# Optimization experiments

Measured on AMD Instinct MI355X. Metric: run time of the kernel, lower is better.

Reference implementation:

```python
import jax, jax.numpy as jnp
from jax import lax
import numpy as np

B = 128
EPS = 1e-5


def _local_conv(x, w, b, kh, kw, sh, sw):
    # x: [B, C, H, W]; w: [nkh, nkw, O, C, kh, kw]; b: [O, nkh, nkw]
    nkh, nkw = w.shape[0], w.shape[1]
    # gather strided patches: [B, C, nkh, nkw, kh, kw]
    pats = jnp.stack([
        jnp.stack([
            x[:, :, di:di + sh * (nkh - 1) + 1:sh, dj:dj + sw * (nkw - 1) + 1:sw]
            for dj in range(kw)], axis=-1)
        for di in range(kh)], axis=-2)
    # per-location (unshared) contraction
    out = jnp.einsum('bchwkl,hwockl->bohw', pats, w)
    return out + b[None]


def _flatten_into_2d(o):
    # [B, O, h, w] -> [B, 1, r*h, r*w] with r = sqrt(O), channel-vector tiled as rxr block
    b, oc, h, w = o.shape
    r = int(round(oc ** 0.5))
    y = o.transpose(0, 2, 3, 1).reshape(b, h, w, r, r)
    y = y.transpose(0, 1, 3, 2, 4).reshape(b, r * h, r * w)
    return y[:, None]


def _layernorm2d(x, g, bta):
    # normalize over last two dims (torch nn.LayerNorm([H, W]))
    m = jnp.mean(x, axis=(-2, -1), keepdims=True)
    v = jnp.mean((x - m) ** 2, axis=(-2, -1), keepdims=True)
    return (x - m) * lax.rsqrt(v + EPS) * g + bta


def _maxpool2(x):
    return lax.reduce_window(x, -jnp.inf, lax.max, (1, 1, 2, 2), (1, 1, 2, 2), 'VALID')


def setup_inputs() -> dict:
    key = jax.random.key(0)
    ks = jax.random.split(key, 5)
    x = jax.random.normal(ks[0], (B, 3, 224, 224), jnp.float32)
    # xavier-normal-ish std for each per-location weight
    w0 = jax.random.normal(ks[1], (55, 55, 16, 3, 8, 8), jnp.float32) * 0.0406
    b0 = jnp.zeros((16, 55, 55), jnp.float32)
    g0 = jnp.ones((220, 220), jnp.float32)
    be0 = jnp.zeros((220, 220), jnp.float32)
    w1 = jax.random.normal(ks[2], (53, 53, 9, 1, 6, 6), jnp.float32) * 0.074
    b1 = jnp.zeros((9, 53, 53), jnp.float32)
    g1 = jnp.ones((159, 159), jnp.float32)
    be1 = jnp.zeros((159, 159), jnp.float32)
    fcw = jax.random.normal(ks[3], (1000, 25281), jnp.float32) * 0.01
    fcb = jnp.zeros((1000,), jnp.float32)
    return {"x": x, "w0": w0, "b0": b0, "g0": g0, "be0": be0,
            "w1": w1, "b1": b1, "g1": g1, "be1": be1, "fcw": fcw, "fcb": fcb}


def reference(x, w0, b0, g0, be0, w1, b1, g1, be1, fcw, fcb):
    # layer 0 (locally connected, padding 0): [B,16,55,55] -> 2D map [B,1,220,220]
    h = _local_conv(x, w0, b0, 8, 8, 4, 4)
    h = _flatten_into_2d(h)
    h = _layernorm2d(jax.nn.relu(h), g0, be0)
    h = _maxpool2(h)  # [B,1,110,110]  (i==0 -> pool; dropout is identity in eval)
    # layer 1: [B,9,53,53] -> [B,1,159,159]; i==1 odd -> no pool
    h = _local_conv(h, w1, b1, 6, 6, 2, 2)
    h = _flatten_into_2d(h)
    h = _layernorm2d(jax.nn.relu(h), g1, be1)
    logits = h.reshape(h.shape[0], -1) @ fcw.T + fcb
    return jax.nn.softmax(logits, axis=1)
```

## Files before the change

kernel.cpp:

```cpp
#include <hip/hip_runtime.h>


typedef __attribute__((ext_vector_type(8))) short short8;
typedef __attribute__((ext_vector_type(4))) float float4v;

__device__ __forceinline__ short f2bf(float f) {
    unsigned u = __float_as_uint(f);
    u += 0x7FFFu + ((u >> 16) & 1u);
    return (short)(u >> 16);
}

__global__ __launch_bounds__(256, 4) void k_conv0(const float* __restrict__ x,
                                                  const float* __restrict__ w0,
                                                  const float* __restrict__ b0,
                                                  float* __restrict__ y0)
{
    __shared__ float xs[2][20 * 132];
    __shared__ float wsd[2][512];

    const int t = threadIdx.x;
    const int orig = blockIdx.x;
    const int xcd = orig & 7, lin = orig >> 3;
    const int bid = (xcd < 2 ? xcd * 97 : 194 + (xcd - 2) * 96) + lin;
    const int tw = bid / 55;
    const int oh = bid % 55;
    const bool lastT = (tw == 13);

    const float* xrow0 = x + (oh << 2) * 224 + (tw << 4);
    const float* wbase = w0 + (oh * 55 + (tw << 2)) * 3072;

    int sb[3], sc[3], gsc[3];
    #pragma unroll
    for (int i = 0; i < 3; ++i) {
        int q = t + (i << 8);
        sb[i] = q / 5;
        sc[i] = q - sb[i] * 5;
        gsc[i] = (lastT && sc[i] > 3) ? 3 : sc[i];
    }
    const int nq = (t < 128) ? 3 : 2;

    const int wlm  = t >> 5;
    const int wom  = (t & 31) >> 1;
    const int whm  = t & 1;
    const bool wact = (t < 128);
    const int wl_l = ((tw << 2) + wlm > 54) ? 0 : wlm;
    const float* wq_base = wbase + wl_l * 3072 + wom * 192 + (whm << 2);

    const int bq = t & 31;
    const int oq = (t >> 5) & 3;
    const int lp = t >> 7;

    float4 xv[3];
    float4 wv = make_float4(0.f, 0.f, 0.f, 0.f);
    #pragma unroll
    for (int i = 0; i < 3; ++i)
        if (i < nq) xv[i] = *(const float4*)(xrow0 + sb[i] * 150528 + (gsc[i] << 2));
    if (wact) wv = *(const float4*)(wq_base);

    float acc[2][4][4] = {};

    #pragma unroll 2
    for (int k = 0; k < 24; ++k) {
        float* xb = xs[k & 1];
        float* wb = wsd[k & 1];
        #pragma unroll
        for (int i = 0; i < 3; ++i) {
            if (i < nq) {
                float* d = xb + (sc[i] << 2) * 132 + sb[i];
                d[0] = xv[i].x; d[132] = xv[i].y; d[264] = xv[i].z; d[396] = xv[i].w;
            }
        }
        if (wact) {
            float* d = wb + (wlm << 7) + (whm << 6) + wom;
            d[0] = wv.x; d[16] = wv.y; d[32] = wv.z; d[48] = wv.w;
        }
        if (k < 23) {
            const int kn = k + 1;
            const int ch = kn >> 3, rw = kn & 7;
            const float* xr = xrow0 + ch * 50176 + rw * 224;
            #pragma unroll
            for (int i = 0; i < 3; ++i)
                if (i < nq) xv[i] = *(const float4*)(xr + sb[i] * 150528 + (gsc[i] << 2));
            if (wact) wv = *(const float4*)(wq_base + (ch << 6) + (rw << 3));
        }
        __syncthreads();
        #pragma unroll
        for (int i = 0; i < 2; ++i) {
            const int l = (lp << 1) + i;
            #pragma unroll
            for (int kc = 0; kc < 8; ++kc) {
                float4 xq = *(const float4*)(xb + ((l << 2) + kc) * 132 + (bq << 2));
                float4 wq = *(const float4*)(wb + (l << 7) + (kc << 4) + (oq << 2));
                const float xr4[4] = {xq.x, xq.y, xq.z, xq.w};
                const float wr4[4] = {wq.x, wq.y, wq.z, wq.w};
                #pragma unroll
                for (int b4 = 0; b4 < 4; ++b4)
                    #pragma unroll
                    for (int j = 0; j < 4; ++j)
                        acc[i][b4][j] += xr4[b4] * wr4[j];
            }
        }
    }

    #pragma unroll
    for (int i = 0; i < 2; ++i) {
        const int l = (lp << 1) + i;
        const int ow = (tw << 2) + l;
        if (ow < 55) {
            const int loc = oh * 55 + ow;
            float bias[4];
            #pragma unroll
            for (int j = 0; j < 4; ++j)
                bias[j] = b0[((oq << 2) + j) * 3025 + loc];
            float* ybase = y0 + ((oh << 2) + oq) * 220 + (ow << 2);
            #pragma unroll
            for (int b4 = 0; b4 < 4; ++b4) {
                const int b = (bq << 2) + b4;
                float ov[4];
                #pragma unroll
                for (int j = 0; j < 4; ++j) {
                    float v = acc[i][b4][j] + bias[j];
                    ov[j] = v > 0.f ? v : 0.f;
                }
                float4 o4;
                o4.x = ov[0]; o4.y = ov[1]; o4.z = ov[2]; o4.w = ov[3];
                *(float4*)(ybase + b * 48400) = o4;
            }
        }
    }
}

__global__ void k_stats(const float* __restrict__ src, float2* __restrict__ stats, int count)
{
    const int b = blockIdx.x, t = threadIdx.x;
    const float* p = src + (long)b * count;
    const int nq = count >> 2;
    float s = 0.f, s2 = 0.f;
    for (int i = t; i < nq; i += 256) {
        float4 v = *(const float4*)(p + (i << 2));
        s  += (v.x + v.y) + (v.z + v.w);
        s2 += (v.x * v.x + v.y * v.y) + (v.z * v.z + v.w * v.w);
    }
    if (t == 0 && (count & 3)) {
        for (int i = nq << 2; i < count; ++i) { float v = p[i]; s += v; s2 += v * v; }
    }
    #pragma unroll
    for (int off = 32; off > 0; off >>= 1) {
        s  += __shfl_down(s,  off, 64);
        s2 += __shfl_down(s2, off, 64);
    }
    __shared__ float rs[4], rs2[4];
    if ((t & 63) == 0) { rs[t >> 6] = s; rs2[t >> 6] = s2; }
    __syncthreads();
    if (t == 0) {
        float S  = rs[0] + rs[1] + rs[2] + rs[3];
        float S2 = rs2[0] + rs2[1] + rs2[2] + rs2[3];
        float m  = S / count;
        float var = S2 / count - m * m;
        stats[b] = make_float2(m, rsqrtf(var + 1e-5f));
    }
}

__global__ void k_pool(const float* __restrict__ y0, const float2* __restrict__ st,
                       const float* __restrict__ g0, const float* __restrict__ be0,
                       float* __restrict__ P)
{
    int idx = blockIdx.x * 256 + threadIdx.x;
    if (idx >= 128 * 110 * 110) return;
    int b = idx / 12100, r = idx % 12100;
    int ph = r / 110, pw = r % 110;
    float2 s = st[b];
    int gb = (ph * 220 + pw) * 2;
    const float* yb = y0 + b * 48400 + gb;
    float2 a0 = *(const float2*)yb;
    float2 a1 = *(const float2*)(yb + 220);
    float2 ga0 = *(const float2*)(g0 + gb),  ga1 = *(const float2*)(g0 + gb + 220);
    float2 ba0 = *(const float2*)(be0 + gb), ba1 = *(const float2*)(be0 + gb + 220);
    float n0 = (a0.x - s.x) * s.y * ga0.x + ba0.x;
    float n1 = (a0.y - s.x) * s.y * ga0.y + ba0.y;
    float n2 = (a1.x - s.x) * s.y * ga1.x + ba1.x;
    float n3 = (a1.y - s.x) * s.y * ga1.y + ba1.y;
    P[idx] = fmaxf(fmaxf(n0, n1), fmaxf(n2, n3));
}

__global__ __launch_bounds__(128) void k_conv1(const float* __restrict__ P,
                                               const float* __restrict__ w1,
                                               const float* __restrict__ b1,
                                               float* __restrict__ y1)
{
    __shared__ float wloc[324];
    __shared__ float pat[128 * 64];
    const int t = threadIdx.x;
    const int loc = blockIdx.x;
    const int oh = loc / 53, ow = loc % 53;
    for (int e = t; e < 324; e += 128) wloc[e] = w1[loc * 324 + e];
    #pragma unroll
    for (int i = 0; i < 9; ++i) {
        int q = t + (i << 7);
        int b_r = q / 9, c = q % 9;
        float pv[4];
        #pragma unroll
        for (int u = 0; u < 4; ++u) {
            int sidx = (c << 2) + u;
            int ki = sidx / 6, kj = sidx % 6;
            pv[u] = P[b_r * 12100 + ((oh << 1) + ki) * 110 + (ow << 1) + kj];
        }
        float4 pq; pq.x = pv[0]; pq.y = pv[1]; pq.z = pv[2]; pq.w = pv[3];
        *(float4*)&pat[(b_r << 6) + ((c ^ (b_r & 15)) << 2)] = pq;
    }
    __syncthreads();
    const int b = t;
    float acc[9];
    #pragma unroll
    for (int o = 0; o < 9; ++o) acc[o] = b1[o * 2809 + loc];
    #pragma unroll
    for (int s4 = 0; s4 < 9; ++s4) {
        float4 pq = *(const float4*)&pat[(b << 6) + ((s4 ^ (b & 15)) << 2)];
        #pragma unroll
        for (int o = 0; o < 9; ++o) {
            float4 wq = *(const float4*)&wloc[o * 36 + (s4 << 2)];
            acc[o] += pq.x * wq.x + pq.y * wq.y + pq.z * wq.z + pq.w * wq.w;
        }
    }
    #pragma unroll
    for (int o = 0; o < 9; ++o) {
        float v = acc[o] > 0.f ? acc[o] : 0.f;
        y1[b * 25281 + (3 * oh + o / 3) * 159 + 3 * ow + o % 3] = v;
    }
}

__global__ void k_normb(const float* __restrict__ y1, const float2* __restrict__ st,
                        const float* __restrict__ g1, const float* __restrict__ be1,
                        unsigned short* __restrict__ hb)
{
    int idx = blockIdx.x * 256 + threadIdx.x;
    int b = idx / 25600, k = idx % 25600;
    float v = 0.f;
    if (k < 25281) {
        float2 s = st[b];
        v = (y1[b * 25281 + k] - s.x) * s.y * g1[k] + be1[k];
    }
    hb[idx] = (unsigned short)f2bf(v);
}

__global__ __launch_bounds__(256) void k_fc_mfma(const unsigned short* __restrict__ hb,
                                                 const float* __restrict__ fcw,
                                                 float* __restrict__ pp)
{
    const int lane = threadIdx.x & 63;
    const int wave = threadIdx.x >> 6;
    const int n0   = (blockIdx.x << 6) + (wave << 4);
    const int k0   = blockIdx.y << 9;
    const int m16  = lane & 15;
    const int q    = lane >> 4;
    const int nc   = n0 + m16;
    const int nrow = nc < 1000 ? nc : 999;
    const long wrow = (long)nrow * 25281;

    float4v acc[8];
    #pragma unroll
    for (int i = 0; i < 8; ++i) acc[i] = (float4v){0.f, 0.f, 0.f, 0.f};

    const unsigned short* ha = hb + m16 * 25600;

    for (int c = 0; c < 16; ++c) {
        const int kb = k0 + (c << 5) + (q << 3);
        long widx = wrow + kb;
        short8 bf;
        if (widx + 8 <= 25281000L) {
            #pragma unroll
            for (int j = 0; j < 8; ++j) bf[j] = f2bf(fcw[widx + j]);
        } else {
            #pragma unroll
            for (int j = 0; j < 8; ++j) {
                long e = widx + j;
                bf[j] = f2bf(e < 25281000L ? fcw[e] : 0.f);
            }
        }
        #pragma unroll
        for (int mt = 0; mt < 8; ++mt) {
            short8 af = *(const short8*)(ha + mt * 16 * 25600 + kb);
            acc[mt] = __builtin_amdgcn_mfma_f32_16x16x32_bf16(af, bf, acc[mt], 0, 0, 0);
        }
    }

    float* prow = pp + ((size_t)blockIdx.y << 17);
    #pragma unroll
    for (int mt = 0; mt < 8; ++mt) {
        const int mb = (mt << 4) + (q << 2);
        #pragma unroll
        for (int i = 0; i < 4; ++i)
            prow[(size_t)(mb + i) * 1024 + nc] = acc[mt][i];
    }
}

__global__ void k_softmax(const float* __restrict__ partials, const float* __restrict__ fcb,
                          float* __restrict__ out)
{
    const int b = blockIdx.x, t = threadIdx.x;
    float v[4];
    float mx = -3.4e38f;
    #pragma unroll
    for (int i = 0; i < 4; ++i) {
        int o = t + (i << 8);
        float s = -3.4e38f;
        if (o < 1000) {
            s = fcb[o];
            for (int bz = 0; bz < 50; ++bz)
                s += partials[(((bz << 7) + b) << 10) + o];
        }
        v[i] = s;
        mx = fmaxf(mx, s);
    }
    __shared__ float red[4], red2[4];
    #pragma unroll
    for (int off = 32; off > 0; off >>= 1) mx = fmaxf(mx, __shfl_down(mx, off, 64));
    if ((t & 63) == 0) red[t >> 6] = mx;
    __syncthreads();
    float M = fmaxf(fmaxf(red[0], red[1]), fmaxf(red[2], red[3]));
    float se = 0.f;
    #pragma unroll
    for (int i = 0; i < 4; ++i) {
        int o = t + (i << 8);
        if (o < 1000) { v[i] = expf(v[i] - M); se += v[i]; }
    }
    #pragma unroll
    for (int off = 32; off > 0; off >>= 1) se += __shfl_down(se, off, 64);
    if ((t & 63) == 0) red2[t >> 6] = se;
    __syncthreads();
    float inv = 1.f / (red2[0] + red2[1] + red2[2] + red2[3]);
    #pragma unroll
    for (int i = 0; i < 4; ++i) {
        int o = t + (i << 8);
        if (o < 1000) out[b * 1000 + o] = v[i] * inv;
    }
}

extern "C" void kernel_launch(void* const* d_in, const int* in_sizes, int n_in,
                              void* d_out, int out_size, void* d_ws, size_t ws_size,
                              hipStream_t stream)
{
    const float* x   = (const float*)d_in[0];
    const float* w0  = (const float*)d_in[1];
    const float* b0  = (const float*)d_in[2];
    const float* g0  = (const float*)d_in[3];
    const float* be0 = (const float*)d_in[4];
    const float* w1  = (const float*)d_in[5];
    const float* b1  = (const float*)d_in[6];
    const float* g1  = (const float*)d_in[7];
    const float* be1 = (const float*)d_in[8];
    const float* fcw = (const float*)d_in[9];
    const float* fcb = (const float*)d_in[10];
    float* out = (float*)d_out;
    float* ws  = (float*)d_ws;

    float*  y0  = ws;
    float2* st0 = (float2*)(ws + 6195200);
    float*  P   = ws + 6195456;
    float*  y1  = ws + 7744256;
    float2* st1 = (float2*)(ws + 10980224);
    unsigned short* hb = (unsigned short*)(ws + 10980480);
    float*  pp  = ws;

    hipLaunchKernelGGL(k_conv0,   dim3(770),     dim3(256), 0, stream, x, w0, b0, y0);
    hipLaunchKernelGGL(k_stats,   dim3(128),     dim3(256), 0, stream, y0, st0, 48400);
    hipLaunchKernelGGL(k_pool,    dim3(6050),    dim3(256), 0, stream, y0, st0, g0, be0, P);
    hipLaunchKernelGGL(k_conv1,   dim3(2809),    dim3(128), 0, stream, P, w1, b1, y1);
    hipLaunchKernelGGL(k_stats,   dim3(128),     dim3(256), 0, stream, y1, st1, 25281);
    hipLaunchKernelGGL(k_normb,   dim3(12800),   dim3(256), 0, stream, y1, st1, g1, be1, hb);
    hipLaunchKernelGGL(k_fc_mfma, dim3(16, 50),  dim3(256), 0, stream, hb, fcw, pp);
    hipLaunchKernelGGL(k_softmax, dim3(128),     dim3(256), 0, stream, pp, fcb, out);
}
```

Baseline: 453.4 us.

## Stage FC weights through LDS with coalesced loads and double buffering

The FC MFMA kernel now loads fp32 weight tiles with coalesced per-k-column reads across 64 rows, converts them to bf16 into a double-buffered shared-memory tile, and prefetches the next 64-wide k-chunk in registers while MFMAs consume the current one. Previously each lane read 8 consecutive floats of its own weight row directly from global memory, which is poorly coalesced. The new path adds LDS traffic, a barrier per chunk and 16 extra registers for the prefetch.

```diff
diff --git a/kernel.cpp b/kernel.cpp
--- a/kernel.cpp
+++ b/kernel.cpp
@@ -247,15 +247,25 @@
                                                  const float* __restrict__ fcw,
                                                  float* __restrict__ pp)
 {
-    const int lane = threadIdx.x & 63;
-    const int wave = threadIdx.x >> 6;
-    const int n0   = (blockIdx.x << 6) + (wave << 4);
+    __shared__ unsigned short bs[2][64 * 72];
+
+    const int t    = threadIdx.x;
+    const int lane = t & 63;
+    const int wave = t >> 6;
+    const int n0b  = blockIdx.x << 6;
     const int k0   = blockIdx.y << 9;
     const int m16  = lane & 15;
     const int q    = lane >> 4;
-    const int nc   = n0 + m16;
-    const int nrow = nc < 1000 ? nc : 999;
-    const long wrow = (long)nrow * 25281;
+    const int nc   = n0b + (wave << 4) + m16;
+
+    const int sk   = t & 63;
+    const int rb   = t >> 6;
+    int srow[16];
+    #pragma unroll
+    for (int i = 0; i < 16; ++i) {
+        int nr = n0b + (i << 2) + rb;
+        srow[i] = nr < 1000 ? nr : 999;
+    }
 
     float4v acc[8];
     #pragma unroll
@@ -263,24 +273,39 @@
 
     const unsigned short* ha = hb + m16 * 25600;
 
-    for (int c = 0; c < 16; ++c) {
-        const int kb = k0 + (c << 5) + (q << 3);
-        long widx = wrow + kb;
-        short8 bf;
-        if (widx + 8 <= 25281000L) {
-            #pragma unroll
-            for (int j = 0; j < 8; ++j) bf[j] = f2bf(fcw[widx + j]);
-        } else {
-            #pragma unroll
-            for (int j = 0; j < 8; ++j) {
-                long e = widx + j;
-                bf[j] = f2bf(e < 25281000L ? fcw[e] : 0.f);
+    float sv[16];
+    {
+        const int gk = k0 + sk;
+        const bool ok = gk < 25281;
+        #pragma unroll
+        for (int i = 0; i < 16; ++i)
+            sv[i] = ok ? fcw[(size_t)srow[i] * 25281 + gk] : 0.f;
+    }
+
+    #pragma unroll 2
+    for (int cc = 0; cc < 8; ++cc) {
+        unsigned short* bb = bs[cc & 1];
+        #pragma unroll
+        for (int i = 0; i < 16; ++i)
+            bb[((i << 2) + rb) * 72 + sk] = (unsigned short)f2bf(sv[i]);
+        if (cc < 7) {
+            const int gk = k0 + ((cc + 1) << 6) + sk;
+            const bool ok = gk < 25281;
+            #pragma unroll
+            for (int i = 0; i < 16; ++i)
+                sv[i] = ok ? fcw[(size_t)srow[i] * 25281 + gk] : 0.f;
+        }
+        __syncthreads();
+        #pragma unroll
+        for (int c2 = 0; c2 < 2; ++c2) {
+            const int klocal = (c2 << 5) + (q << 3);
+            short8 bf = *(const short8*)&bb[((wave << 4) + m16) * 72 + klocal];
+            const int kb = k0 + (cc << 6) + klocal;
+            #pragma unroll
+            for (int mt = 0; mt < 8; ++mt) {
+                short8 af = *(const short8*)(ha + mt * 16 * 25600 + kb);
+                acc[mt] = __builtin_amdgcn_mfma_f32_16x16x32_bf16(af, bf, acc[mt], 0, 0, 0);
             }
-        }
-        #pragma unroll
-        for (int mt = 0; mt < 8; ++mt) {
-            short8 af = *(const short8*)(ha + mt * 16 * 25600 + kb);
-            acc[mt] = __builtin_amdgcn_mfma_f32_16x16x32_bf16(af, bf, acc[mt], 0, 0, 0);
         }
     }
 
```

After: 443.1 us. 2.3% less time.
